# Optimization experiments

Measured on AMD Instinct MI355X. Metric: run time of the kernel, lower is better.

Reference implementation:

```python
import jax, jax.numpy as jnp
import numpy as np


def _interp_linear_align_corners(w, new_len):
    """Linear (bilinear with trivial 2nd axis) interpolation along last axis,
    align_corners=True, matching torch F.interpolate. w: (..., k) -> (..., new_len)."""
    k = w.shape[-1]
    scale = (k - 1) / (new_len - 1) if new_len > 1 else 0.0
    pos = jnp.arange(new_len, dtype=w.dtype) * jnp.asarray(scale, w.dtype)
    lo = jnp.floor(pos).astype(jnp.int32)
    hi = jnp.minimum(lo + 1, k - 1)
    frac = pos - lo.astype(w.dtype)
    return w[..., lo] * (1.0 - frac) + w[..., hi] * frac


def _depthwise_conv(x, kernel, pad_h, pad_w):
    # x: (B,C,H,W), kernel: (C,1,Kh,Kw), groups=C
    C = x.shape[1]
    return jax.lax.conv_general_dilated(
        x, kernel, window_strides=(1, 1),
        padding=[(pad_h, pad_h), (pad_w, pad_w)],
        dimension_numbers=("NCHW", "OIHW", "NCHW"),
        feature_group_count=C)


def setup_inputs() -> dict:
    key = jax.random.key(0)
    k1, k2, k3, k4, k5 = jax.random.split(key, 5)
    dim, ksize = 128, 13
    B, H, W = 32, 64, 64
    fan = 1.0 / np.sqrt(ksize)  # torch Conv2d default init scale (groups=dim -> fan_in=k)
    return {
        "x": jax.random.normal(k1, (B, dim, H, W), dtype=jnp.float32),
        "h_weight": jax.random.uniform(k2, (dim, 1, ksize, 1), jnp.float32, -fan, fan),
        "w_weight": jax.random.uniform(k3, (dim, 1, 1, ksize), jnp.float32, -fan, fan),
        "h_bias": jax.random.uniform(k4, (dim,), jnp.float32, -fan, fan),
        "w_bias": jax.random.uniform(k5, (dim,), jnp.float32, -fan, fan),
    }


def reference(x, h_weight, w_weight, h_bias, w_bias):
    B, C, H, W = x.shape
    Kh, Kw = 2 * H - 1, 2 * W - 1
    # Interpolate base kernels to instance kernel sizes (align_corners=True bilinear,
    # degenerate to 1-D linear since the other spatial dim has size 1).
    hk = _interp_linear_align_corners(h_weight[:, :, :, 0], Kh)[..., None]   # (C,1,Kh,1)
    wk = _interp_linear_align_corners(w_weight[:, :, 0, :], Kw)[:, :, None]  # (C,1,1,Kw)
    y = _depthwise_conv(x, hk, H - 1, 0) + h_bias[None, :, None, None]
    y = _depthwise_conv(y, wk, 0, W - 1) + w_bias[None, :, None, None]
    return y
```

## Files before the change

kernel.cpp:

```cpp
#include <hip/hip_runtime.h>


#define STRB 72

typedef short  bfrag  __attribute__((ext_vector_type(8)));
typedef float  f32x4  __attribute__((ext_vector_type(4)));
typedef unsigned short us4 __attribute__((ext_vector_type(4)));

__device__ __forceinline__ unsigned short f2bf(float f) {
    unsigned u = __builtin_bit_cast(unsigned, f);
    u += 0x7fffu + ((u >> 16) & 1u);
    return (unsigned short)(u >> 16);
}

__device__ __forceinline__ void lds_barrier() {
    asm volatile("s_waitcnt lgkmcnt(0)" ::: "memory");
    __builtin_amdgcn_s_barrier();
}

__global__ __launch_bounds__(256, 4)
void oversize_conv_v5(const float* __restrict__ x,
                      const float* __restrict__ hwt,
                      const float* __restrict__ wwt,
                      const float* __restrict__ hb,
                      const float* __restrict__ wb,
                      float* __restrict__ out)
{
    __shared__ __align__(16) unsigned short Xs[64 * STRB];
    __shared__ __align__(16) unsigned short Aw[64 * STRB];
    __shared__ __align__(16) unsigned short Ah[64 * STRB];
    __shared__ __align__(16) unsigned short PT[64 * STRB];
    __shared__ float hk[128], wk[128], swp[256];
    __shared__ __align__(16) float sw[64];

    const int tid = threadIdx.x;
    const int c   = blockIdx.x & 127;
    const int g4  = blockIdx.x >> 7;
    const size_t imgStride = (size_t)128 * 4096;
    const size_t img0 = ((size_t)(4 * g4) * 128 + c) * 4096;

    const int wv = tid >> 6, lane = tid & 63;
    const int r = lane & 15, gq = lane >> 4;

    float4 xv[4];
    {
        const float4* xg = (const float4*)(x + img0);
        #pragma unroll
        for (int q = 0; q < 4; ++q) xv[q] = xg[tid + q * 256];
    }

    if (tid < 127) {
        const float scale = 12.0f / 126.0f;
        float pos = (float)tid * scale;
        int   lo  = (int)pos;
        float fr  = pos - (float)lo;
        int   hi  = (lo + 1 < 12) ? lo + 1 : 12;
        hk[tid] = hwt[c * 13 + lo] * (1.0f - fr) + hwt[c * 13 + hi] * fr;
        wk[tid] = wwt[c * 13 + lo] * (1.0f - fr) + wwt[c * 13 + hi] * fr;
    }
    lds_barrier();

    {
        const int row = tid >> 2;
        const int cb  = (tid & 3) * 16;
        #pragma unroll
        for (int q = 0; q < 4; ++q) {
            us4 vh, vw;
            #pragma unroll
            for (int j = 0; j < 4; ++j) {
                int col = cb + q * 4 + j;
                vh[j] = f2bf(hk[col - row + 63]);
                vw[j] = f2bf(wk[col - row + 63]);
            }
            *(us4*)&Ah[row * STRB + cb + q * 4] = vh;
            *(us4*)&Aw[row * STRB + cb + q * 4] = vw;
        }
    }
    {
        const int ow = tid >> 2, q = tid & 3;
        float s = 0.f;
        #pragma unroll
        for (int i = 0; i < 16; ++i) s += wk[(q * 16 + i) - ow + 63];
        swp[tid] = s;
    }
    #pragma unroll
    for (int q = 0; q < 4; ++q) {
        int idx = tid + q * 256;
        int row = idx >> 4;
        int col = (idx & 15) * 4;
        us4 v;
        v[0] = f2bf(xv[q].x); v[1] = f2bf(xv[q].y);
        v[2] = f2bf(xv[q].z); v[3] = f2bf(xv[q].w);
        *(us4*)&Xs[row * STRB + col] = v;
    }
    float4 xn[4];
    {
        const float4* xg = (const float4*)(x + img0 + imgStride);
        #pragma unroll
        for (int q = 0; q < 4; ++q) xn[q] = xg[tid + q * 256];
    }
    lds_barrier();

    if (tid < 64)
        sw[tid] = swp[4 * tid] + swp[4 * tid + 1] + swp[4 * tid + 2] + swp[4 * tid + 3];

    const float hbc = hb[c], wbc = wb[c];

    #pragma unroll
    for (int i = 0; i < 4; ++i) {
        bfrag a0 = *(const bfrag*)&Xs[(16 * wv + r) * STRB + 8 * gq];
        bfrag a1 = *(const bfrag*)&Xs[(16 * wv + r) * STRB + 32 + 8 * gq];
        f32x4 acc[4] = {};
        #pragma unroll
        for (int nt = 0; nt < 4; ++nt) {
            bfrag b0 = *(const bfrag*)&Aw[(16 * nt + r) * STRB + 8 * gq];
            bfrag b1 = *(const bfrag*)&Aw[(16 * nt + r) * STRB + 32 + 8 * gq];
            acc[nt] = __builtin_amdgcn_mfma_f32_16x16x32_bf16(a0, b0, acc[nt], 0, 0, 0);
            acc[nt] = __builtin_amdgcn_mfma_f32_16x16x32_bf16(a1, b1, acc[nt], 0, 0, 0);
        }
        #pragma unroll
        for (int nt = 0; nt < 4; ++nt) {
            us4 p;
            p[0] = f2bf(acc[nt][0]); p[1] = f2bf(acc[nt][1]);
            p[2] = f2bf(acc[nt][2]); p[3] = f2bf(acc[nt][3]);
            *(us4*)&PT[(16 * nt + r) * STRB + 16 * wv + 4 * gq] = p;
        }
        lds_barrier();

        f32x4 sw4 = *(const f32x4*)&sw[16 * wv + 4 * gq];
        f32x4 bias;
        bias[0] = hbc * sw4[0] + wbc; bias[1] = hbc * sw4[1] + wbc;
        bias[2] = hbc * sw4[2] + wbc; bias[3] = hbc * sw4[3] + wbc;

        bfrag pa0 = *(const bfrag*)&PT[(16 * wv + r) * STRB + 8 * gq];
        bfrag pa1 = *(const bfrag*)&PT[(16 * wv + r) * STRB + 32 + 8 * gq];
        f32x4 acc2[4] = {bias, bias, bias, bias};
        #pragma unroll
        for (int nt = 0; nt < 4; ++nt) {
            bfrag bh0 = *(const bfrag*)&Ah[(16 * nt + r) * STRB + 8 * gq];
            bfrag bh1 = *(const bfrag*)&Ah[(16 * nt + r) * STRB + 32 + 8 * gq];
            acc2[nt] = __builtin_amdgcn_mfma_f32_16x16x32_bf16(pa0, bh0, acc2[nt], 0, 0, 0);
            acc2[nt] = __builtin_amdgcn_mfma_f32_16x16x32_bf16(pa1, bh1, acc2[nt], 0, 0, 0);
        }

        if (i < 3) {
            #pragma unroll
            for (int q = 0; q < 4; ++q) {
                int idx = tid + q * 256;
                int row = idx >> 4;
                int col = (idx & 15) * 4;
                us4 v;
                v[0] = f2bf(xn[q].x); v[1] = f2bf(xn[q].y);
                v[2] = f2bf(xn[q].z); v[3] = f2bf(xn[q].w);
                *(us4*)&Xs[row * STRB + col] = v;
            }
        }
        if (i < 2) {
            const float4* xg = (const float4*)(x + img0 + (size_t)(i + 2) * imgStride);
            #pragma unroll
            for (int q = 0; q < 4; ++q) xn[q] = xg[tid + q * 256];
        }

        {
            float* og = out + img0 + (size_t)i * imgStride;
            #pragma unroll
            for (int nt = 0; nt < 4; ++nt) {
                __builtin_nontemporal_store(
                    acc2[nt],
                    (f32x4*)&og[(size_t)(16 * nt + r) * 64 + 16 * wv + 4 * gq]);
            }
        }

        lds_barrier();
    }
}

extern "C" void kernel_launch(void* const* d_in, const int* in_sizes, int n_in,
                              void* d_out, int out_size, void* d_ws, size_t ws_size,
                              hipStream_t stream)
{
    const float* x   = (const float*)d_in[0];
    const float* hwt = (const float*)d_in[1];
    const float* wwt = (const float*)d_in[2];
    const float* hb  = (const float*)d_in[3];
    const float* wb  = (const float*)d_in[4];
    oversize_conv_v5<<<1024, 256, 0, stream>>>(x, hwt, wwt, hb, wb, (float*)d_out);
}
```

Measured before the change: 30.43 us.

## Compress Toeplitz weight tiles in LDS and process two images per block

```diff
diff --git a/kernel.cpp b/kernel.cpp
--- a/kernel.cpp
+++ b/kernel.cpp
@@ -2,6 +2,7 @@
 
 
 #define STRB 72
+#define MSTR 120
 
 typedef short  bfrag  __attribute__((ext_vector_type(8)));
 typedef float  f32x4  __attribute__((ext_vector_type(4)));
@@ -12,14 +13,18 @@
     u += 0x7fffu + ((u >> 16) & 1u);
     return (unsigned short)(u >> 16);
 }
+__device__ __forceinline__ float bf2f(unsigned short h) {
+    unsigned u = ((unsigned)h) << 16;
+    return __builtin_bit_cast(float, u);
+}
 
 __device__ __forceinline__ void lds_barrier() {
     asm volatile("s_waitcnt lgkmcnt(0)" ::: "memory");
     __builtin_amdgcn_s_barrier();
 }
 
-__global__ __launch_bounds__(256, 4)
-void oversize_conv_v5(const float* __restrict__ x,
+__global__ __launch_bounds__(256, 6)
+void oversize_conv_v7(const float* __restrict__ x,
                       const float* __restrict__ hwt,
                       const float* __restrict__ wwt,
                       const float* __restrict__ hb,
@@ -27,17 +32,17 @@
                       float* __restrict__ out)
 {
     __shared__ __align__(16) unsigned short Xs[64 * STRB];
-    __shared__ __align__(16) unsigned short Aw[64 * STRB];
-    __shared__ __align__(16) unsigned short Ah[64 * STRB];
     __shared__ __align__(16) unsigned short PT[64 * STRB];
-    __shared__ float hk[128], wk[128], swp[256];
+    __shared__ __align__(16) unsigned short Mw[16 * MSTR];
+    __shared__ __align__(16) unsigned short Mh[16 * MSTR];
+    __shared__ unsigned short hkb[128], wkb[128];
     __shared__ __align__(16) float sw[64];
 
     const int tid = threadIdx.x;
-    const int c   = blockIdx.x & 127;
-    const int g4  = blockIdx.x >> 7;
+    const int c    = blockIdx.x & 127;
+    const int pair = blockIdx.x >> 7;
     const size_t imgStride = (size_t)128 * 4096;
-    const size_t img0 = ((size_t)(4 * g4) * 128 + c) * 4096;
+    const size_t img0 = ((size_t)(2 * pair) * 128 + c) * 4096;
 
     const int wv = tid >> 6, lane = tid & 63;
     const int r = lane & 15, gq = lane >> 4;
@@ -55,33 +60,23 @@
         int   lo  = (int)pos;
         float fr  = pos - (float)lo;
         int   hi  = (lo + 1 < 12) ? lo + 1 : 12;
-        hk[tid] = hwt[c * 13 + lo] * (1.0f - fr) + hwt[c * 13 + hi] * fr;
-        wk[tid] = wwt[c * 13 + lo] * (1.0f - fr) + wwt[c * 13 + hi] * fr;
+        hkb[tid] = f2bf(hwt[c * 13 + lo] * (1.0f - fr) + hwt[c * 13 + hi] * fr);
+        wkb[tid] = f2bf(wwt[c * 13 + lo] * (1.0f - fr) + wwt[c * 13 + hi] * fr);
     }
     lds_barrier();
 
-    {
-        const int row = tid >> 2;
-        const int cb  = (tid & 3) * 16;
-        #pragma unroll
-        for (int q = 0; q < 4; ++q) {
-            us4 vh, vw;
-            #pragma unroll
-            for (int j = 0; j < 4; ++j) {
-                int col = cb + q * 4 + j;
-                vh[j] = f2bf(hk[col - row + 63]);
-                vw[j] = f2bf(wk[col - row + 63]);
-            }
-            *(us4*)&Ah[row * STRB + cb + q * 4] = vh;
-            *(us4*)&Aw[row * STRB + cb + q * 4] = vw;
-        }
+    for (int k = tid; k < 16 * 112; k += 256) {
+        int rr  = k / 112;
+        int col = k - rr * 112;
+        int t   = col + 15 - rr;
+        Mw[rr * MSTR + col] = wkb[t];
+        Mh[rr * MSTR + col] = hkb[t];
     }
-    {
-        const int ow = tid >> 2, q = tid & 3;
+    if (tid < 64) {
         float s = 0.f;
-        #pragma unroll
-        for (int i = 0; i < 16; ++i) s += wk[(q * 16 + i) - ow + 63];
-        swp[tid] = s;
+        #pragma unroll 8
+        for (int iw = 0; iw < 64; ++iw) s += bf2f(wkb[iw - tid + 63]);
+        sw[tid] = s;
     }
     #pragma unroll
     for (int q = 0; q < 4; ++q) {
@@ -101,20 +96,22 @@
     }
     lds_barrier();
 
-    if (tid < 64)
-        sw[tid] = swp[4 * tid] + swp[4 * tid + 1] + swp[4 * tid + 2] + swp[4 * tid + 3];
-
     const float hbc = hb[c], wbc = wb[c];
+    f32x4 sw4 = *(const f32x4*)&sw[16 * wv + 4 * gq];
+    f32x4 bias;
+    bias[0] = hbc * sw4[0] + wbc; bias[1] = hbc * sw4[1] + wbc;
+    bias[2] = hbc * sw4[2] + wbc; bias[3] = hbc * sw4[3] + wbc;
 
     #pragma unroll
-    for (int i = 0; i < 4; ++i) {
+    for (int i = 0; i < 2; ++i) {
         bfrag a0 = *(const bfrag*)&Xs[(16 * wv + r) * STRB + 8 * gq];
         bfrag a1 = *(const bfrag*)&Xs[(16 * wv + r) * STRB + 32 + 8 * gq];
         f32x4 acc[4] = {};
         #pragma unroll
         for (int nt = 0; nt < 4; ++nt) {
-            bfrag b0 = *(const bfrag*)&Aw[(16 * nt + r) * STRB + 8 * gq];
-            bfrag b1 = *(const bfrag*)&Aw[(16 * nt + r) * STRB + 32 + 8 * gq];
+            const int mb = r * MSTR + 8 * gq - 16 * nt + 48;
+            bfrag b0 = *(const bfrag*)&Mw[mb];
+            bfrag b1 = *(const bfrag*)&Mw[mb + 32];
             acc[nt] = __builtin_amdgcn_mfma_f32_16x16x32_bf16(a0, b0, acc[nt], 0, 0, 0);
             acc[nt] = __builtin_amdgcn_mfma_f32_16x16x32_bf16(a1, b1, acc[nt], 0, 0, 0);
         }
@@ -127,23 +124,19 @@
         }
         lds_barrier();
 
-        f32x4 sw4 = *(const f32x4*)&sw[16 * wv + 4 * gq];
-        f32x4 bias;
-        bias[0] = hbc * sw4[0] + wbc; bias[1] = hbc * sw4[1] + wbc;
-        bias[2] = hbc * sw4[2] + wbc; bias[3] = hbc * sw4[3] + wbc;
-
         bfrag pa0 = *(const bfrag*)&PT[(16 * wv + r) * STRB + 8 * gq];
         bfrag pa1 = *(const bfrag*)&PT[(16 * wv + r) * STRB + 32 + 8 * gq];
         f32x4 acc2[4] = {bias, bias, bias, bias};
         #pragma unroll
         for (int nt = 0; nt < 4; ++nt) {
-            bfrag bh0 = *(const bfrag*)&Ah[(16 * nt + r) * STRB + 8 * gq];
-            bfrag bh1 = *(const bfrag*)&Ah[(16 * nt + r) * STRB + 32 + 8 * gq];
+            const int mb = r * MSTR + 8 * gq - 16 * nt + 48;
+            bfrag bh0 = *(const bfrag*)&Mh[mb];
+            bfrag bh1 = *(const bfrag*)&Mh[mb + 32];
             acc2[nt] = __builtin_amdgcn_mfma_f32_16x16x32_bf16(pa0, bh0, acc2[nt], 0, 0, 0);
             acc2[nt] = __builtin_amdgcn_mfma_f32_16x16x32_bf16(pa1, bh1, acc2[nt], 0, 0, 0);
         }
 
-        if (i < 3) {
+        if (i == 0) {
             #pragma unroll
             for (int q = 0; q < 4; ++q) {
                 int idx = tid + q * 256;
@@ -155,19 +148,13 @@
                 *(us4*)&Xs[row * STRB + col] = v;
             }
         }
-        if (i < 2) {
-            const float4* xg = (const float4*)(x + img0 + (size_t)(i + 2) * imgStride);
-            #pragma unroll
-            for (int q = 0; q < 4; ++q) xn[q] = xg[tid + q * 256];
-        }
 
         {
             float* og = out + img0 + (size_t)i * imgStride;
             #pragma unroll
             for (int nt = 0; nt < 4; ++nt) {
-                __builtin_nontemporal_store(
-                    acc2[nt],
-                    (f32x4*)&og[(size_t)(16 * nt + r) * 64 + 16 * wv + 4 * gq]);
+                f32x4 v = acc2[nt];
+                *(f32x4*)&og[(size_t)(16 * nt + r) * 64 + 16 * wv + 4 * gq] = v;
             }
         }
 
@@ -184,5 +171,5 @@
     const float* wwt = (const float*)d_in[2];
     const float* hb  = (const float*)d_in[3];
     const float* wb  = (const float*)d_in[4];
-    oversize_conv_v5<<<1024, 256, 0, stream>>>(x, hwt, wwt, hb, wb, (float*)d_out);
+    oversize_conv_v7<<<2048, 256, 0, stream>>>(x, hwt, wwt, hb, wb, (float*)d_out);
 }
```

Measured after the change: 27.24 us. 1.12x faster.
